# Performance work log

Measured on AMD Instinct MI355X. Metric: run time of the kernel, lower is better.

## Reference

```python
import jax, jax.numpy as jnp
import numpy as np

T, B, OBS, H, P, L, A = 512, 128, 512, 256, 128, 4, 4


def _ln(x, scale, bias, eps=1e-6):
    mu = jnp.mean(x, axis=-1, keepdims=True)
    var = jnp.mean((x - mu) ** 2, axis=-1, keepdims=True)
    return (x - mu) * jax.lax.rsqrt(var + eps) * scale + bias


def _binop(qi, qj):
    # S5 reset-aware associative operator: elements (A, b, reset_flag)
    Ai, bi, ci = qi
    Aj, bj, cj = qj
    A = (Aj * Ai) * (1.0 - cj) + Aj * cj
    b = (Aj * bi + bj) * (1.0 - cj) + bj * cj
    c = ci * (1.0 - cj) + cj
    return A, b, c


def _s5_layer(x, dones, h0, scale, bias, lam_re, lam_im, b_re, b_im, c_re, c_im, d_vec, log_step, glu_W, glu_b):
    # x: (T,B,H) real, dones: (T,B), h0: (B,P) complex64
    skip = x
    u = _ln(x, scale, bias)                                  # prenorm
    lam = lam_re + 1j * lam_im                               # (P,)
    step = jnp.exp(log_step)                                 # (P,)
    lam_bar = jnp.exp(lam * step)                            # ZOH discretization
    B_bar = ((lam_bar - 1.0) / lam)[:, None] * (b_re + 1j * b_im)  # (P,H)
    Bu = jnp.einsum('tbh,ph->tbp', u.astype(jnp.complex64), B_bar)  # (T,B,P)
    A_el = jnp.concatenate([jnp.ones((1, B, P), jnp.complex64),
                            jnp.broadcast_to(lam_bar.astype(jnp.complex64), (T, B, P))], axis=0)
    b_el = jnp.concatenate([h0[None], Bu], axis=0)
    c_el = jnp.concatenate([jnp.zeros((1, B, 1), jnp.float32), dones[..., None]], axis=0)
    _, xs, _ = jax.lax.associative_scan(_binop, (A_el, b_el, c_el), axis=0)
    xs = xs[1:]                                              # (T,B,P) complex states
    new_h = xs[-1]
    C = c_re + 1j * c_im                                     # (H,P)
    ys = 2.0 * jnp.real(jnp.einsum('tbp,hp->tbh', xs, C)) + d_vec * u  # conj_sym output + D*u
    z = _ln(ys, scale, bias)                                 # gtrxl norm (shared LayerNorm params)
    z = jax.nn.gelu(z)                                       # half_glu1
    z = z * jax.nn.sigmoid(z @ glu_W + glu_b)
    return skip + z, new_h


def setup_inputs() -> dict:
    key = jax.random.key(0)
    ks = jax.random.split(key, 40)
    f32 = jnp.float32

    def n(i, shape, s=1.0):
        return jax.random.normal(ks[i], shape, f32) * s

    inp = {}
    inp['obs'] = n(0, (T, B, OBS))
    inp['dones'] = (jax.random.uniform(ks[1], (T, B)) < 0.01).astype(f32)
    inp['hidden_re'] = jnp.zeros((L, B, P), f32)
    inp['hidden_im'] = jnp.zeros((L, B, P), f32)
    inp['enc0_W'] = n(2, (OBS, 128), 1.0 / np.sqrt(OBS))
    inp['enc0_b'] = jnp.zeros((128,), f32)
    inp['enc1_W'] = n(3, (128, H), 1.0 / np.sqrt(128))
    inp['enc1_b'] = jnp.zeros((H,), f32)
    inp['norm_scale'] = jnp.ones((L, H), f32)
    inp['norm_bias'] = jnp.zeros((L, H), f32)
    inp['Lambda_re'] = -0.5 * jax.random.uniform(ks[4], (L, P), f32) - 0.1
    inp['Lambda_im'] = n(5, (L, P), np.pi)
    inp['B_re'] = n(6, (L, P, H), 1.0 / np.sqrt(H))
    inp['B_im'] = n(7, (L, P, H), 1.0 / np.sqrt(H))
    inp['C_re'] = n(8, (L, H, P), 1.0 / np.sqrt(2 * P))
    inp['C_im'] = n(9, (L, H, P), 1.0 / np.sqrt(2 * P))
    inp['D'] = n(10, (L, H))
    inp['log_step'] = jax.random.uniform(ks[11], (L, P), f32, np.log(1e-3), np.log(1e-1))
    inp['glu_W'] = n(12, (L, H, H), 1.0 / np.sqrt(H))
    inp['glu_b'] = jnp.zeros((L, H), f32)
    inp['ab0_W'] = n(13, (H, 128), 1.0 / np.sqrt(H))
    inp['ab0_b'] = jnp.zeros((128,), f32)
    inp['ab1_W'] = n(14, (128, 128), 1.0 / np.sqrt(128))
    inp['ab1_b'] = jnp.zeros((128,), f32)
    inp['adec_W'] = n(15, (128, A), 0.01 / np.sqrt(128))
    inp['adec_b'] = jnp.full((A,), 0.5, f32)
    inp['log_std'] = jnp.full((A,), -0.7, f32)
    inp['vb0_W'] = n(16, (H, 128), 1.0 / np.sqrt(H))
    inp['vb0_b'] = jnp.zeros((128,), f32)
    inp['vb1_W'] = n(17, (128, 128), 1.0 / np.sqrt(128))
    inp['vb1_b'] = jnp.zeros((128,), f32)
    inp['vdec_W'] = n(18, (128, 1), 1.0 / np.sqrt(128))
    inp['vdec_b'] = jnp.zeros((1,), f32)
    return inp


def reference(obs, dones, hidden_re, hidden_im, enc0_W, enc0_b, enc1_W, enc1_b,
              norm_scale, norm_bias, Lambda_re, Lambda_im, B_re, B_im, C_re, C_im,
              D, log_step, glu_W, glu_b, ab0_W, ab0_b, ab1_W, ab1_b, adec_W, adec_b,
              log_std, vb0_W, vb0_b, vb1_W, vb1_b, vdec_W, vdec_b):
    e = jax.nn.leaky_relu(obs @ enc0_W + enc0_b)
    e = jax.nn.leaky_relu(e @ enc1_W + enc1_b)
    h0 = (hidden_re + 1j * hidden_im).astype(jnp.complex64)  # (L,B,P)
    new_h = []
    for l in range(L):
        e, hl = _s5_layer(e, dones, h0[l], norm_scale[l], norm_bias[l],
                          Lambda_re[l], Lambda_im[l], B_re[l], B_im[l],
                          C_re[l], C_im[l], D[l], log_step[l], glu_W[l], glu_b[l])
        new_h.append(hl)
    new_h = jnp.stack(new_h)
    am = jax.nn.leaky_relu(e @ ab0_W + ab0_b)
    am = jax.nn.leaky_relu(am @ ab1_W + ab1_b)
    am = am @ adec_W + adec_b                                # actor mean (T,B,A)
    v = jax.nn.leaky_relu(e @ vb0_W + vb0_b)
    v = jax.nn.leaky_relu(v @ vb1_W + vb1_b)
    v = v @ vdec_W + vdec_b                                  # critic (T,B,1)
    sc = jnp.broadcast_to(jnp.exp(log_std), am.shape)        # Normal scale (pi params)
    out = jnp.concatenate([am, sc, v], axis=-1)              # (T,B,2A+1)
    return out, jnp.real(new_h), jnp.imag(new_h)
```

## Files before the change

kernel.cpp:

```cpp
#include <hip/hip_runtime.h>
#include <math.h>

#define TT 512
#define BB 128
#define OBSD 512
#define HD 256
#define PD 128
#define LD 4
#define NTB (TT*BB)

typedef __bf16 bf16x8 __attribute__((ext_vector_type(8)));
typedef float  f32x4  __attribute__((ext_vector_type(4)));

__device__ __forceinline__ float bf2f(unsigned short u) {
    return __uint_as_float(((unsigned)u) << 16);
}
__device__ __forceinline__ unsigned short f2bf(float f) {
    unsigned u = __float_as_uint(f);
    unsigned r = (u + 0x7FFFu + ((u >> 16) & 1u)) >> 16;
    return (unsigned short)r;
}
__device__ __forceinline__ float gelu_f(float x) {
    float x3 = x * x * x;
    return 0.5f * x * (1.f + tanhf(0.7978845608028654f * (x + 0.044715f * x3)));
}

template<int MODE, int NJ, int NK>
__global__ __launch_bounds__(512) void mgemm2(
    const unsigned short* __restrict__ A, const unsigned short* __restrict__ BT,
    int LDA, const float* __restrict__ bias,
    const float* __restrict__ lnsc, const float* __restrict__ lnbi,
    const unsigned short* __restrict__ aux1, unsigned short* Xio,
    unsigned short* __restrict__ U, int wU)
{
    constexpr int NJW = NJ / 2;
    constexpr int LPS = 2 + NJW;
    constexpr int K = NK * 32;
    const int N = NJ * 64;
    __shared__ unsigned short smA[3 * 2048];
    __shared__ unsigned short smB[3 * NJ * 2048];
    float2 (*red)[8] = reinterpret_cast<float2(*)[8]>(&smA[0]);
    int tid = threadIdx.x;
    int lane = tid & 63, w = tid >> 6;
    int m16 = lane & 15, quad = lane >> 4;
    int m0 = blockIdx.x * 64;

    f32x4 acc[4][NJW] = {};

    auto stage = [&](int slot, int kt) {
        int k0 = kt << 5;
#pragma unroll
        for (int j = 0; j < 2; ++j) {
            int chunk = w * 2 + j;
            int e = chunk * 128 + lane * 2;
            int row = e >> 5, kb = e & 31;
            const unsigned short* g = A + (size_t)(m0 + row) * LDA + k0 + kb;
            __builtin_amdgcn_global_load_lds(
                (const __attribute__((address_space(1))) void*)g,
                (__attribute__((address_space(3))) void*)(smA + slot * 2048 + e), 4, 0, 0);
        }
#pragma unroll
        for (int j = 0; j < NJW; ++j) {
            int chunk = w * NJW + j;
            int e = chunk * 512 + lane * 8;
            int p = e >> 11, r = (e >> 5) & 63, kq = e & 31;
            const unsigned short* g = BT + (size_t)(p * 64 + r) * K + k0 + kq;
            __builtin_amdgcn_global_load_lds(
                (const __attribute__((address_space(1))) void*)g,
                (__attribute__((address_space(3))) void*)(smB + slot * NJ * 2048 + e), 16, 0, 0);
        }
    };

    int nk = NK;
    stage(0, 0);
    stage(1, 1);
    int cur = 0, nxt = 2;
    for (int t = 0; t < nk; ++t) {
        int rem = nk - 1 - t;
        if (rem >= 2) {
            stage(nxt, t + 2);
            nxt = (nxt == 2) ? 0 : nxt + 1;
            asm volatile("s_waitcnt vmcnt(%0)" :: "i"(2 * LPS) : "memory");
        } else if (rem == 1) {
            asm volatile("s_waitcnt vmcnt(%0)" :: "i"(LPS) : "memory");
        } else {
            asm volatile("s_waitcnt vmcnt(0)" ::: "memory");
        }
        __builtin_amdgcn_s_barrier();
        __builtin_amdgcn_sched_barrier(0);
        bf16x8 af[4], bfr[NJW];
#pragma unroll
        for (int mi = 0; mi < 4; ++mi)
            af[mi] = *(const bf16x8*)(smA + cur * 2048 + (mi * 16 + m16) * 32 + quad * 8);
#pragma unroll
        for (int nj = 0; nj < NJW; ++nj)
            bfr[nj] = *(const bf16x8*)(smB + cur * NJ * 2048 + (w * NJW + nj) * 512 + m16 * 32 + quad * 8);
#pragma unroll
        for (int mi = 0; mi < 4; ++mi)
#pragma unroll
            for (int nj = 0; nj < NJW; ++nj)
                acc[mi][nj] = __builtin_amdgcn_mfma_f32_16x16x32_bf16(
                    bfr[nj], af[mi], acc[mi][nj], 0, 0, 0);
        __builtin_amdgcn_sched_barrier(0);
        __builtin_amdgcn_s_barrier();
        cur = (cur == 2) ? 0 : cur + 1;
    }

    int colb = w * (NJW * 16) + quad * 4;

    if (MODE == 1) {
#pragma unroll
        for (int mi = 0; mi < 4; ++mi) {
            size_t rowb = (size_t)(m0 + mi * 16 + m16) * N;
#pragma unroll
            for (int nj = 0; nj < NJW; ++nj) {
                ushort4 o = { f2bf(acc[mi][nj][0]), f2bf(acc[mi][nj][1]),
                              f2bf(acc[mi][nj][2]), f2bf(acc[mi][nj][3]) };
                *(ushort4*)(U + rowb + colb + nj * 16) = o;
            }
        }
        return;
    }

#pragma unroll
    for (int mi = 0; mi < 4; ++mi) {
        size_t rowb = (size_t)(m0 + mi * 16 + m16) * N;
        float s = 0.f, q = 0.f;
#pragma unroll
        for (int nj = 0; nj < NJW; ++nj) {
            float4 bn = *(const float4*)(bias + colb + nj * 16);
            ushort4 a1, xo;
            if (MODE == 2 || MODE == 3) a1 = *(const ushort4*)(aux1 + rowb + colb + nj * 16);
            if (MODE == 3)              xo = *(const ushort4*)(Xio + rowb + colb + nj * 16);
            float vv[4];
#pragma unroll
            for (int r = 0; r < 4; ++r) {
                float v = acc[mi][nj][r];
                float bv = (r == 0) ? bn.x : (r == 1) ? bn.y : (r == 2) ? bn.z : bn.w;
                if (MODE == 0) {
                    v += bv; v = v > 0.f ? v : 0.01f * v;
                } else if (MODE == 2) {
                    float u = bf2f(r == 0 ? a1.x : r == 1 ? a1.y : r == 2 ? a1.z : a1.w);
                    v += bv * u;
                } else if (MODE == 3) {
                    float zz = bf2f(r == 0 ? a1.x : r == 1 ? a1.y : r == 2 ? a1.z : a1.w);
                    float xx = bf2f(r == 0 ? xo.x : r == 1 ? xo.y : r == 2 ? xo.z : xo.w);
                    float sg = 1.f / (1.f + expf(-(v + bv)));
                    v = xx + zz * sg;
                }
                vv[r] = v;
                acc[mi][nj][r] = v;
                s += v; q += v * v;
            }
            if (MODE == 0 || MODE == 3) {
                ushort4 o = { f2bf(vv[0]), f2bf(vv[1]), f2bf(vv[2]), f2bf(vv[3]) };
                *(ushort4*)(Xio + rowb + colb + nj * 16) = o;
            }
        }
        if (MODE != 3 || wU) {
            s += __shfl_xor(s, 16); q += __shfl_xor(q, 16);
            s += __shfl_xor(s, 32); q += __shfl_xor(q, 32);
            if (quad == 0) red[mi * 16 + m16][w] = float2{s, q};
        }
    }
    if (MODE == 3 && !wU) return;
    __syncthreads();

#pragma unroll
    for (int mi = 0; mi < 4; ++mi) {
        int row_l = mi * 16 + m16;
        float S = 0.f, Q = 0.f;
#pragma unroll
        for (int ww = 0; ww < 8; ++ww) {
            float2 tv = red[row_l][ww];
            S += tv.x; Q += tv.y;
        }
        float mu = S * (1.f / 256.f);
        float var = Q * (1.f / 256.f) - mu * mu;
        float rstd = rsqrtf(var + 1e-6f);
        size_t rowb = (size_t)(m0 + row_l) * N;
#pragma unroll
        for (int nj = 0; nj < NJW; ++nj) {
            float4 ls = *(const float4*)(lnsc + colb + nj * 16);
            float4 lb = *(const float4*)(lnbi + colb + nj * 16);
            float o[4];
#pragma unroll
            for (int r = 0; r < 4; ++r) {
                float sc = (r == 0) ? ls.x : (r == 1) ? ls.y : (r == 2) ? ls.z : ls.w;
                float bi = (r == 0) ? lb.x : (r == 1) ? lb.y : (r == 2) ? lb.z : lb.w;
                float v = (acc[mi][nj][r] - mu) * rstd * sc + bi;
                if (MODE == 2) v = gelu_f(v);
                o[r] = v;
            }
            ushort4 ov = { f2bf(o[0]), f2bf(o[1]), f2bf(o[2]), f2bf(o[3]) };
            *(ushort4*)(U + rowb + colb + nj * 16) = ov;
        }
    }
}

__global__ __launch_bounds__(512) void glu_bu_k(
    const unsigned short* __restrict__ Z,
    const unsigned short* __restrict__ GT,
    const unsigned short* __restrict__ BT2,
    const float* __restrict__ glub,
    const float* __restrict__ ns2, const float* __restrict__ nb2,
    unsigned short* __restrict__ Xio,
    unsigned short* __restrict__ Uo,
    unsigned short* __restrict__ BUo)
{
    const int N = 256;
    __shared__ unsigned short smA[2 * 2048];
    __shared__ unsigned short smB[2 * 8192];
    __shared__ unsigned short zbuf[64 * 264];
    float2 (*red)[8] = reinterpret_cast<float2(*)[8]>(&smA[0]);
    int tid = threadIdx.x;
    int lane = tid & 63, w = tid >> 6;
    int m16 = lane & 15, quad = lane >> 4;
    int m0 = blockIdx.x * 64;
    int colb = w * 32 + quad * 4;

    f32x4 acc[4][2] = {};

    auto stage1 = [&](int slot, int kt) {
        int k0 = kt << 5;
#pragma unroll
        for (int j = 0; j < 2; ++j) {
            int e = (w * 2 + j) * 128 + lane * 2;
            int row = e >> 5, kb = e & 31;
            const unsigned short* g = Z + (size_t)(m0 + row) * 256 + k0 + kb;
            __builtin_amdgcn_global_load_lds(
                (const __attribute__((address_space(1))) void*)g,
                (__attribute__((address_space(3))) void*)(smA + slot * 2048 + e), 4, 0, 0);
        }
#pragma unroll
        for (int j = 0; j < 2; ++j) {
            int e = (w * 2 + j) * 512 + lane * 8;
            int p = e >> 11, r = (e >> 5) & 63, kq = e & 31;
            const unsigned short* g = GT + (size_t)(p * 64 + r) * 256 + k0 + kq;
            __builtin_amdgcn_global_load_lds(
                (const __attribute__((address_space(1))) void*)g,
                (__attribute__((address_space(3))) void*)(smB + slot * 8192 + e), 16, 0, 0);
        }
    };
    auto stage2 = [&](int slot, int kt) {
        int k0 = kt << 5;
#pragma unroll
        for (int j = 0; j < 2; ++j) {
            int e = (w * 2 + j) * 512 + lane * 8;
            int p = e >> 11, r = (e >> 5) & 63, kq = e & 31;
            const unsigned short* g = BT2 + (size_t)(p * 64 + r) * 256 + k0 + kq;
            __builtin_amdgcn_global_load_lds(
                (const __attribute__((address_space(1))) void*)g,
                (__attribute__((address_space(3))) void*)(smB + slot * 8192 + e), 16, 0, 0);
        }
    };

    stage1(0, 0);
    for (int t = 0; t < 8; ++t) {
        int cur = t & 1;
        if (t + 1 < 8) {
            stage1(cur ^ 1, t + 1);
            asm volatile("s_waitcnt vmcnt(4)" ::: "memory");
        } else {
            asm volatile("s_waitcnt vmcnt(0)" ::: "memory");
        }
        __builtin_amdgcn_s_barrier();
        __builtin_amdgcn_sched_barrier(0);
        bf16x8 af[4], bfr[2];
#pragma unroll
        for (int mi = 0; mi < 4; ++mi)
            af[mi] = *(const bf16x8*)(smA + cur * 2048 + (mi * 16 + m16) * 32 + quad * 8);
#pragma unroll
        for (int nj = 0; nj < 2; ++nj)
            bfr[nj] = *(const bf16x8*)(smB + cur * 8192 + (w * 2 + nj) * 512 + m16 * 32 + quad * 8);
#pragma unroll
        for (int mi = 0; mi < 4; ++mi)
#pragma unroll
            for (int nj = 0; nj < 2; ++nj)
                acc[mi][nj] = __builtin_amdgcn_mfma_f32_16x16x32_bf16(
                    bfr[nj], af[mi], acc[mi][nj], 0, 0, 0);
        __builtin_amdgcn_sched_barrier(0);
        __builtin_amdgcn_s_barrier();
    }

    stage2(0, 0);

#pragma unroll
    for (int mi = 0; mi < 4; ++mi) {
        int row_l = mi * 16 + m16;
        size_t rowb = (size_t)(m0 + row_l) * N;
        float s = 0.f, q = 0.f;
#pragma unroll
        for (int nj = 0; nj < 2; ++nj) {
            float4 gb = *(const float4*)(glub + colb + nj * 16);
            ushort4 a1 = *(const ushort4*)(Z + rowb + colb + nj * 16);
            ushort4 xo = *(const ushort4*)(Xio + rowb + colb + nj * 16);
            float vv[4];
#pragma unroll
            for (int r = 0; r < 4; ++r) {
                float v = acc[mi][nj][r];
                float bv = (r == 0) ? gb.x : (r == 1) ? gb.y : (r == 2) ? gb.z : gb.w;
                float zz = bf2f(r == 0 ? a1.x : r == 1 ? a1.y : r == 2 ? a1.z : a1.w);
                float xx = bf2f(r == 0 ? xo.x : r == 1 ? xo.y : r == 2 ? xo.z : xo.w);
                float sg = 1.f / (1.f + expf(-(v + bv)));
                v = xx + zz * sg;
                vv[r] = v;
                acc[mi][nj][r] = v;
                s += v; q += v * v;
            }
            ushort4 o = { f2bf(vv[0]), f2bf(vv[1]), f2bf(vv[2]), f2bf(vv[3]) };
            *(ushort4*)(Xio + rowb + colb + nj * 16) = o;
        }
        s += __shfl_xor(s, 16); q += __shfl_xor(q, 16);
        s += __shfl_xor(s, 32); q += __shfl_xor(q, 32);
        if (quad == 0) red[row_l][w] = float2{s, q};
    }
    __syncthreads();

#pragma unroll
    for (int mi = 0; mi < 4; ++mi) {
        int row_l = mi * 16 + m16;
        float S = 0.f, Q = 0.f;
#pragma unroll
        for (int ww = 0; ww < 8; ++ww) { float2 tv = red[row_l][ww]; S += tv.x; Q += tv.y; }
        float mu = S * (1.f / 256.f);
        float var = Q * (1.f / 256.f) - mu * mu;
        float rstd = rsqrtf(var + 1e-6f);
        size_t rowb = (size_t)(m0 + row_l) * N;
#pragma unroll
        for (int nj = 0; nj < 2; ++nj) {
            float4 ls = *(const float4*)(ns2 + colb + nj * 16);
            float4 lb = *(const float4*)(nb2 + colb + nj * 16);
            float o[4];
#pragma unroll
            for (int r = 0; r < 4; ++r) {
                float sc = (r == 0) ? ls.x : (r == 1) ? ls.y : (r == 2) ? ls.z : ls.w;
                float bi = (r == 0) ? lb.x : (r == 1) ? lb.y : (r == 2) ? lb.z : lb.w;
                o[r] = (acc[mi][nj][r] - mu) * rstd * sc + bi;
            }
            ushort4 ov = { f2bf(o[0]), f2bf(o[1]), f2bf(o[2]), f2bf(o[3]) };
            *(ushort4*)(Uo + rowb + colb + nj * 16) = ov;
            *(ushort4*)(zbuf + row_l * 264 + colb + nj * 16) = ov;
        }
    }
    __syncthreads();

    f32x4 acc2[4][2] = {};
    for (int t = 0; t < 8; ++t) {
        int cur = t & 1;
        if (t + 1 < 8) {
            stage2(cur ^ 1, t + 1);
            asm volatile("s_waitcnt vmcnt(2)" ::: "memory");
        } else {
            asm volatile("s_waitcnt vmcnt(0)" ::: "memory");
        }
        __builtin_amdgcn_s_barrier();
        __builtin_amdgcn_sched_barrier(0);
        bf16x8 af[4], bfr[2];
#pragma unroll
        for (int mi = 0; mi < 4; ++mi)
            af[mi] = *(const bf16x8*)(zbuf + (mi * 16 + m16) * 264 + t * 32 + quad * 8);
#pragma unroll
        for (int nj = 0; nj < 2; ++nj)
            bfr[nj] = *(const bf16x8*)(smB + cur * 8192 + (w * 2 + nj) * 512 + m16 * 32 + quad * 8);
#pragma unroll
        for (int mi = 0; mi < 4; ++mi)
#pragma unroll
            for (int nj = 0; nj < 2; ++nj)
                acc2[mi][nj] = __builtin_amdgcn_mfma_f32_16x16x32_bf16(
                    bfr[nj], af[mi], acc2[mi][nj], 0, 0, 0);
        __builtin_amdgcn_sched_barrier(0);
        __builtin_amdgcn_s_barrier();
    }
#pragma unroll
    for (int mi = 0; mi < 4; ++mi) {
        size_t rowb = (size_t)(m0 + mi * 16 + m16) * N;
#pragma unroll
        for (int nj = 0; nj < 2; ++nj) {
            ushort4 o = { f2bf(acc2[mi][nj][0]), f2bf(acc2[mi][nj][1]),
                          f2bf(acc2[mi][nj][2]), f2bf(acc2[mi][nj][3]) };
            *(ushort4*)(BUo + rowb + colb + nj * 16) = o;
        }
    }
}

__global__ __launch_bounds__(512) void head_fused_k(
    const unsigned short* __restrict__ Xp, const unsigned short* __restrict__ W0T,
    const float* __restrict__ cb0,
    const unsigned short* __restrict__ AB1T, const unsigned short* __restrict__ VB1T,
    const float* __restrict__ ab1b, const float* __restrict__ vb1b,
    const float* __restrict__ adW, const float* __restrict__ adb,
    const float* __restrict__ lstd,
    const float* __restrict__ vdW, const float* __restrict__ vdb,
    float* __restrict__ out)
{
    __shared__ unsigned short smA[2 * 2048];
    __shared__ unsigned short smB[2 * 8192];
    __shared__ unsigned short zbuf[64 * 264];
    float (*redh)[8][4] = reinterpret_cast<float(*)[8][4]>(&smA[0]);
    int tid = threadIdx.x;
    int lane = tid & 63, w = tid >> 6;
    int m16 = lane & 15, quad = lane >> 4;
    int m0 = blockIdx.x * 64;
    int colb = w * 32 + quad * 4;

    f32x4 acc[4][2] = {};

    auto stage1 = [&](int slot, int kt) {
        int k0 = kt << 5;
#pragma unroll
        for (int j = 0; j < 2; ++j) {
            int e = (w * 2 + j) * 128 + lane * 2;
            int row = e >> 5, kb = e & 31;
            const unsigned short* g = Xp + (size_t)(m0 + row) * 256 + k0 + kb;
            __builtin_amdgcn_global_load_lds(
                (const __attribute__((address_space(1))) void*)g,
                (__attribute__((address_space(3))) void*)(smA + slot * 2048 + e), 4, 0, 0);
        }
#pragma unroll
        for (int j = 0; j < 2; ++j) {
            int e = (w * 2 + j) * 512 + lane * 8;
            int p = e >> 11, r = (e >> 5) & 63, kq = e & 31;
            const unsigned short* g = W0T + (size_t)(p * 64 + r) * 256 + k0 + kq;
            __builtin_amdgcn_global_load_lds(
                (const __attribute__((address_space(1))) void*)g,
                (__attribute__((address_space(3))) void*)(smB + slot * 8192 + e), 16, 0, 0);
        }
    };
    auto stage2 = [&](int slot, int kt) {
        int k0 = kt << 5;
#pragma unroll
        for (int j = 0; j < 2; ++j) {
            int e = (w * 2 + j) * 512 + lane * 8;
            int r = e >> 5, kq = e & 31;
            const unsigned short* g = (r < 128)
                ? AB1T + (size_t)r * 128 + k0 + kq
                : VB1T + (size_t)(r - 128) * 128 + k0 + kq;
            __builtin_amdgcn_global_load_lds(
                (const __attribute__((address_space(1))) void*)g,
                (__attribute__((address_space(3))) void*)(smB + slot * 8192 + e), 16, 0, 0);
        }
    };

    stage1(0, 0);
    for (int t = 0; t < 8; ++t) {
        int cur = t & 1;
        if (t + 1 < 8) {
            stage1(cur ^ 1, t + 1);
            asm volatile("s_waitcnt vmcnt(4)" ::: "memory");
        } else {
            asm volatile("s_waitcnt vmcnt(0)" ::: "memory");
        }
        __builtin_amdgcn_s_barrier();
        __builtin_amdgcn_sched_barrier(0);
        bf16x8 af[4], bfr[2];
#pragma unroll
        for (int mi = 0; mi < 4; ++mi)
            af[mi] = *(const bf16x8*)(smA + cur * 2048 + (mi * 16 + m16) * 32 + quad * 8);
#pragma unroll
        for (int nj = 0; nj < 2; ++nj)
            bfr[nj] = *(const bf16x8*)(smB + cur * 8192 + (w * 2 + nj) * 512 + m16 * 32 + quad * 8);
#pragma unroll
        for (int mi = 0; mi < 4; ++mi)
#pragma unroll
            for (int nj = 0; nj < 2; ++nj)
                acc[mi][nj] = __builtin_amdgcn_mfma_f32_16x16x32_bf16(
                    bfr[nj], af[mi], acc[mi][nj], 0, 0, 0);
        __builtin_amdgcn_sched_barrier(0);
        __builtin_amdgcn_s_barrier();
    }
    stage2(0, 0);
#pragma unroll
    for (int mi = 0; mi < 4; ++mi) {
        int row_l = mi * 16 + m16;
#pragma unroll
        for (int nj = 0; nj < 2; ++nj) {
            float4 bn = *(const float4*)(cb0 + colb + nj * 16);
            float v0 = acc[mi][nj][0] + bn.x; v0 = v0 > 0.f ? v0 : 0.01f * v0;
            float v1 = acc[mi][nj][1] + bn.y; v1 = v1 > 0.f ? v1 : 0.01f * v1;
            float v2 = acc[mi][nj][2] + bn.z; v2 = v2 > 0.f ? v2 : 0.01f * v2;
            float v3 = acc[mi][nj][3] + bn.w; v3 = v3 > 0.f ? v3 : 0.01f * v3;
            ushort4 o = { f2bf(v0), f2bf(v1), f2bf(v2), f2bf(v3) };
            *(ushort4*)(zbuf + row_l * 264 + colb + nj * 16) = o;
        }
    }
    __syncthreads();

    f32x4 acc2[4][2] = {};
    int abase = (w < 4) ? 0 : 128;
    for (int t = 0; t < 4; ++t) {
        int cur = t & 1;
        if (t + 1 < 4) {
            stage2(cur ^ 1, t + 1);
            asm volatile("s_waitcnt vmcnt(2)" ::: "memory");
        } else {
            asm volatile("s_waitcnt vmcnt(0)" ::: "memory");
        }
        __builtin_amdgcn_s_barrier();
        __builtin_amdgcn_sched_barrier(0);
        bf16x8 af[4], bfr[2];
#pragma unroll
        for (int mi = 0; mi < 4; ++mi)
            af[mi] = *(const bf16x8*)(zbuf + (mi * 16 + m16) * 264 + abase + t * 32 + quad * 8);
#pragma unroll
// ... 182 lines not shown
            float nhr = fmaf(s.x, hr, fmaf(-s.y, hi, s.z));
            float nhi = fmaf(s.x, hi, fmaf(s.y, hr, s.w));
            hr = nhr; hi = nhi;
        }
        outre[gid] = hr; outim[gid] = hi;
    }
    __syncthreads();
    float hr = shin[chunk][pl].x, hi = shin[chunk][pl].y;
#pragma unroll
    for (int j = 0; j < 32; ++j) {
        unsigned v = buf[j];
        float bur = bf2f((unsigned short)(v & 0xFFFFu));
        float bui = bf2f((unsigned short)(v >> 16));
        float nr, ni;
        if (sdone[t0 + j] != 0.f) { nr = bur; ni = bui; }
        else {
            nr = fmaf(ar, hr, fmaf(-ai, hi, bur));
            ni = fmaf(ar, hi, fmaf(ai, hr, bui));
        }
        hr = nr; hi = ni;
        size_t off = ((size_t)(t0 + j) * BB + b) * 256 + 2 * p;
        *(unsigned*)(xs + off) = ((unsigned)f2bf(ni) << 16) | f2bf(nr);
    }
}

__global__ __launch_bounds__(256) void prep_k(
    const float* __restrict__ Br, const float* __restrict__ Bi,
    const float* __restrict__ Cr, const float* __restrict__ Ci,
    const float* __restrict__ Lr, const float* __restrict__ Li,
    const float* __restrict__ ls, unsigned short* bbarT, unsigned short* ccatT)
{
    int gid = blockIdx.x * 256 + threadIdx.x;
    int l = gid >> 15;
    int rem = gid & 32767;
    int p = rem >> 8;
    int h = rem & 255;
    float lr = Lr[l * PD + p], li = Li[l * PD + p];
    float st = expf(ls[l * PD + p]);
    float er = expf(lr * st);
    float lbr = er * cosf(li * st);
    float lbi = er * sinf(li * st);
    float nr = lbr - 1.f, ni = lbi;
    float den = lr * lr + li * li;
    float fr = (nr * lr + ni * li) / den;
    float fi = (ni * lr - nr * li) / den;
    float bre = Br[(size_t)(l * PD + p) * HD + h];
    float bim = Bi[(size_t)(l * PD + p) * HD + h];
    size_t lb = (size_t)l * 65536;
    bbarT[lb + (size_t)(2 * p) * 256 + h]     = f2bf(fr * bre - fi * bim);
    bbarT[lb + (size_t)(2 * p + 1) * 256 + h] = f2bf(fr * bim + fi * bre);
    float cre = Cr[(size_t)(l * HD + h) * PD + p];
    float cim = Ci[(size_t)(l * HD + h) * PD + p];
    ccatT[lb + (size_t)h * 256 + 2 * p]     = f2bf(2.f * cre);
    ccatT[lb + (size_t)h * 256 + 2 * p + 1] = f2bf(-2.f * cim);
}

__global__ __launch_bounds__(256) void tcvt_k(const float* __restrict__ in,
    unsigned short* __restrict__ out, int K, int N)
{
    int gid = blockIdx.x * 256 + threadIdx.x;
    if (gid >= K * N) return;
    int k = gid / N, n = gid - k * N;
    out[(size_t)n * K + k] = f2bf(in[gid]);
}

__global__ __launch_bounds__(256) void tcvt4_k(const float* __restrict__ in,
    unsigned short* __restrict__ out)
{
    int gid = blockIdx.x * 256 + threadIdx.x;
    int l = gid >> 16;
    int rem = gid & 65535;
    int k = rem >> 8, n = rem & 255;
    out[(size_t)l * 65536 + (size_t)n * 256 + k] = f2bf(in[gid]);
}

__global__ __launch_bounds__(256) void catb_k(const float* __restrict__ a,
    const float* __restrict__ b, float* __restrict__ out)
{
    int i = threadIdx.x;
    out[i] = (i < 128) ? a[i] : b[i - 128];
}

extern "C" void kernel_launch(void* const* d_in, const int* in_sizes, int n_in,
                              void* d_out, int out_size, void* d_ws, size_t ws_size,
                              hipStream_t stream) {
    (void)in_sizes; (void)n_in; (void)out_size; (void)ws_size;
    const float* obs     = (const float*)d_in[0];
    const float* dones   = (const float*)d_in[1];
    const float* hre     = (const float*)d_in[2];
    const float* him     = (const float*)d_in[3];
    const float* enc0_W  = (const float*)d_in[4];
    const float* enc0_b  = (const float*)d_in[5];
    const float* enc1_W  = (const float*)d_in[6];
    const float* enc1_b  = (const float*)d_in[7];
    const float* nsc     = (const float*)d_in[8];
    const float* nbi     = (const float*)d_in[9];
    const float* Lre     = (const float*)d_in[10];
    const float* Lim     = (const float*)d_in[11];
    const float* B_re    = (const float*)d_in[12];
    const float* B_im    = (const float*)d_in[13];
    const float* C_re    = (const float*)d_in[14];
    const float* C_im    = (const float*)d_in[15];
    const float* Dv      = (const float*)d_in[16];
    const float* lstep   = (const float*)d_in[17];
    const float* glu_W   = (const float*)d_in[18];
    const float* glu_b   = (const float*)d_in[19];
    const float* ab0_W   = (const float*)d_in[20];
    const float* ab0_b   = (const float*)d_in[21];
    const float* ab1_W   = (const float*)d_in[22];
    const float* ab1_b   = (const float*)d_in[23];
    const float* adec_W  = (const float*)d_in[24];
    const float* adec_b  = (const float*)d_in[25];
    const float* log_std = (const float*)d_in[26];
    const float* vb0_W   = (const float*)d_in[27];
    const float* vb0_b   = (const float*)d_in[28];
    const float* vb1_W   = (const float*)d_in[29];
    const float* vb1_b   = (const float*)d_in[30];
    const float* vdec_W  = (const float*)d_in[31];
    const float* vdec_b  = (const float*)d_in[32];

    const size_t MB = (size_t)1 << 20;
    char* wsb = (char*)d_ws;
    unsigned short* XS    = (unsigned short*)(wsb);
    unsigned short* U1    = (unsigned short*)(wsb + 64 * MB);
    unsigned short* X     = (unsigned short*)(wsb + 96 * MB);
    unsigned short* U     = (unsigned short*)(wsb + 128 * MB);
    unsigned short* BU    = (unsigned short*)(wsb + 160 * MB);
    char* wgt = wsb + 192 * MB;
    unsigned short* BBART = (unsigned short*)(wgt);
    unsigned short* CCATT = (unsigned short*)(wgt + 512 * 1024);
    unsigned short* GLUT  = (unsigned short*)(wgt + 1024 * 1024);
    unsigned short* E0T   = (unsigned short*)(wgt + 1536 * 1024);
    unsigned short* E1T   = (unsigned short*)(wgt + 1664 * 1024);
    unsigned short* AB0VT = (unsigned short*)(wgt + 1728 * 1024);
    unsigned short* AB1T  = (unsigned short*)(wgt + 1856 * 1024);
    unsigned short* VB1T  = (unsigned short*)(wgt + 1888 * 1024);
    float*          CB0   = (float*)(wgt + 1920 * 1024);

    float* out   = (float*)d_out;
    float* outre = out + (size_t)NTB * 9;
    float* outim = outre + LD * BB * PD;

    prep_k<<<512, 256, 0, stream>>>(B_re, B_im, C_re, C_im, Lre, Lim, lstep, BBART, CCATT);
    tcvt_k<<<256, 256, 0, stream>>>(enc0_W, E0T, 512, 128);
    tcvt_k<<<128, 256, 0, stream>>>(enc1_W, E1T, 128, 256);
    tcvt4_k<<<1024, 256, 0, stream>>>(glu_W, GLUT);
    tcvt_k<<<128, 256, 0, stream>>>(ab0_W, AB0VT, 256, 128);
    tcvt_k<<<128, 256, 0, stream>>>(vb0_W, AB0VT + 128 * 256, 256, 128);
    tcvt_k<<<64, 256, 0, stream>>>(ab1_W, AB1T, 128, 128);
    tcvt_k<<<64, 256, 0, stream>>>(vb1_W, VB1T, 128, 128);
    catb_k<<<1, 256, 0, stream>>>(ab0_b, vb0_b, CB0);

    mgemm_obs<<<1024, 256, 0, stream>>>(obs, E0T, U1, enc0_b);
    mgemm2<0, 4, 4><<<1024, 512, 0, stream>>>(U1, E1T, 128, enc1_b, nsc, nbi, nullptr, X, U, 1);

    mgemm2<1, 4, 8><<<1024, 512, 0, stream>>>(U, BBART, 256,
                                           nullptr, nullptr, nullptr, nullptr, nullptr, BU, 0);
    for (int l = 0; l < LD; ++l) {
        scan2_k<<<512, 512, 0, stream>>>(BU, XS, dones, hre + l * BB * PD, him + l * BB * PD,
                                         Lre + l * PD, Lim + l * PD, lstep + l * PD,
                                         outre + l * BB * PD, outim + l * BB * PD);
        mgemm2<2, 4, 8><<<1024, 512, 0, stream>>>(XS, CCATT + (size_t)l * 65536, 256,
                                               Dv + l * HD, nsc + l * HD, nbi + l * HD, U, nullptr, U, 1);
        if (l + 1 < LD) {
            glu_bu_k<<<1024, 512, 0, stream>>>(U, GLUT + (size_t)l * 65536,
                                               BBART + (size_t)(l + 1) * 65536,
                                               glu_b + l * HD,
                                               nsc + (l + 1) * HD, nbi + (l + 1) * HD,
                                               X, U, BU);
        } else {
            mgemm2<3, 4, 8><<<1024, 512, 0, stream>>>(U, GLUT + (size_t)l * 65536, 256,
                                               glu_b + l * HD, nsc, nbi, U, X, U, 0);
        }
    }

    head_fused_k<<<1024, 512, 0, stream>>>(X, AB0VT, CB0, AB1T, VB1T, ab1_b, vb1_b,
                                           adec_W, adec_b, log_std, vdec_W, vdec_b, out);
}
```

Measured before the change: 872.4 us.

## Fuse C-projection, GLU and next-layer Bu GEMMs into one per-layer kernel

Each S5 layer now runs a single layer_k kernel that chains three GEMMs: the C output projection with D*u, LayerNorm and GELU, then the GLU gate with the residual, then the next layer's prenorm LayerNorm and the B_bar input projection. Intermediates stay in LDS (zbuf) between GEMMs instead of going through global memory. The encoder's second layer is fused the same way with the first Bu projection. This removes several kernel launches and a global round-trip of the normalized activations per layer, but each block now runs longer serial GEMM chains, which may lower occupancy because of the larger LDS footprint.

Result: slower. 927.0 us (+6.3%).

```diff
diff --git a/kernel.cpp b/kernel.cpp
--- a/kernel.cpp
+++ b/kernel.cpp
@@ -25,183 +25,16 @@
     return 0.5f * x * (1.f + tanhf(0.7978845608028654f * (x + 0.044715f * x3)));
 }
 
-template<int MODE, int NJ, int NK>
-__global__ __launch_bounds__(512) void mgemm2(
-    const unsigned short* __restrict__ A, const unsigned short* __restrict__ BT,
-    int LDA, const float* __restrict__ bias,
-    const float* __restrict__ lnsc, const float* __restrict__ lnbi,
-    const unsigned short* __restrict__ aux1, unsigned short* Xio,
-    unsigned short* __restrict__ U, int wU)
-{
-    constexpr int NJW = NJ / 2;
-    constexpr int LPS = 2 + NJW;
-    constexpr int K = NK * 32;
-    const int N = NJ * 64;
-    __shared__ unsigned short smA[3 * 2048];
-    __shared__ unsigned short smB[3 * NJ * 2048];
-    float2 (*red)[8] = reinterpret_cast<float2(*)[8]>(&smA[0]);
-    int tid = threadIdx.x;
-    int lane = tid & 63, w = tid >> 6;
-    int m16 = lane & 15, quad = lane >> 4;
-    int m0 = blockIdx.x * 64;
-
-    f32x4 acc[4][NJW] = {};
-
-    auto stage = [&](int slot, int kt) {
-        int k0 = kt << 5;
-#pragma unroll
-        for (int j = 0; j < 2; ++j) {
-            int chunk = w * 2 + j;
-            int e = chunk * 128 + lane * 2;
-            int row = e >> 5, kb = e & 31;
-            const unsigned short* g = A + (size_t)(m0 + row) * LDA + k0 + kb;
-            __builtin_amdgcn_global_load_lds(
-                (const __attribute__((address_space(1))) void*)g,
-                (__attribute__((address_space(3))) void*)(smA + slot * 2048 + e), 4, 0, 0);
-        }
-#pragma unroll
-        for (int j = 0; j < NJW; ++j) {
-            int chunk = w * NJW + j;
-            int e = chunk * 512 + lane * 8;
-            int p = e >> 11, r = (e >> 5) & 63, kq = e & 31;
-            const unsigned short* g = BT + (size_t)(p * 64 + r) * K + k0 + kq;
-            __builtin_amdgcn_global_load_lds(
-                (const __attribute__((address_space(1))) void*)g,
-                (__attribute__((address_space(3))) void*)(smB + slot * NJ * 2048 + e), 16, 0, 0);
-        }
-    };
-
-    int nk = NK;
-    stage(0, 0);
-    stage(1, 1);
-    int cur = 0, nxt = 2;
-    for (int t = 0; t < nk; ++t) {
-        int rem = nk - 1 - t;
-        if (rem >= 2) {
-            stage(nxt, t + 2);
-            nxt = (nxt == 2) ? 0 : nxt + 1;
-            asm volatile("s_waitcnt vmcnt(%0)" :: "i"(2 * LPS) : "memory");
-        } else if (rem == 1) {
-            asm volatile("s_waitcnt vmcnt(%0)" :: "i"(LPS) : "memory");
-        } else {
-            asm volatile("s_waitcnt vmcnt(0)" ::: "memory");
-        }
-        __builtin_amdgcn_s_barrier();
-        __builtin_amdgcn_sched_barrier(0);
-        bf16x8 af[4], bfr[NJW];
-#pragma unroll
-        for (int mi = 0; mi < 4; ++mi)
-            af[mi] = *(const bf16x8*)(smA + cur * 2048 + (mi * 16 + m16) * 32 + quad * 8);
-#pragma unroll
-        for (int nj = 0; nj < NJW; ++nj)
-            bfr[nj] = *(const bf16x8*)(smB + cur * NJ * 2048 + (w * NJW + nj) * 512 + m16 * 32 + quad * 8);
-#pragma unroll
-        for (int mi = 0; mi < 4; ++mi)
-#pragma unroll
-            for (int nj = 0; nj < NJW; ++nj)
-                acc[mi][nj] = __builtin_amdgcn_mfma_f32_16x16x32_bf16(
-                    bfr[nj], af[mi], acc[mi][nj], 0, 0, 0);
-        __builtin_amdgcn_sched_barrier(0);
-        __builtin_amdgcn_s_barrier();
-        cur = (cur == 2) ? 0 : cur + 1;
-    }
-
-    int colb = w * (NJW * 16) + quad * 4;
-
-    if (MODE == 1) {
-#pragma unroll
-        for (int mi = 0; mi < 4; ++mi) {
-            size_t rowb = (size_t)(m0 + mi * 16 + m16) * N;
-#pragma unroll
-            for (int nj = 0; nj < NJW; ++nj) {
-                ushort4 o = { f2bf(acc[mi][nj][0]), f2bf(acc[mi][nj][1]),
-                              f2bf(acc[mi][nj][2]), f2bf(acc[mi][nj][3]) };
-                *(ushort4*)(U + rowb + colb + nj * 16) = o;
-            }
-        }
-        return;
-    }
-
-#pragma unroll
-    for (int mi = 0; mi < 4; ++mi) {
-        size_t rowb = (size_t)(m0 + mi * 16 + m16) * N;
-        float s = 0.f, q = 0.f;
-#pragma unroll
-        for (int nj = 0; nj < NJW; ++nj) {
-            float4 bn = *(const float4*)(bias + colb + nj * 16);
-            ushort4 a1, xo;
-            if (MODE == 2 || MODE == 3) a1 = *(const ushort4*)(aux1 + rowb + colb + nj * 16);
-            if (MODE == 3)              xo = *(const ushort4*)(Xio + rowb + colb + nj * 16);
-            float vv[4];
-#pragma unroll
-            for (int r = 0; r < 4; ++r) {
-                float v = acc[mi][nj][r];
-                float bv = (r == 0) ? bn.x : (r == 1) ? bn.y : (r == 2) ? bn.z : bn.w;
-                if (MODE == 0) {
-                    v += bv; v = v > 0.f ? v : 0.01f * v;
-                } else if (MODE == 2) {
-                    float u = bf2f(r == 0 ? a1.x : r == 1 ? a1.y : r == 2 ? a1.z : a1.w);
-                    v += bv * u;
-                } else if (MODE == 3) {
-                    float zz = bf2f(r == 0 ? a1.x : r == 1 ? a1.y : r == 2 ? a1.z : a1.w);
-                    float xx = bf2f(r == 0 ? xo.x : r == 1 ? xo.y : r == 2 ? xo.z : xo.w);
-                    float sg = 1.f / (1.f + expf(-(v + bv)));
-                    v = xx + zz * sg;
-                }
-                vv[r] = v;
-                acc[mi][nj][r] = v;
-                s += v; q += v * v;
-            }
-            if (MODE == 0 || MODE == 3) {
-                ushort4 o = { f2bf(vv[0]), f2bf(vv[1]), f2bf(vv[2]), f2bf(vv[3]) };
-                *(ushort4*)(Xio + rowb + colb + nj * 16) = o;
-            }
-        }
-        if (MODE != 3 || wU) {
-            s += __shfl_xor(s, 16); q += __shfl_xor(q, 16);
-            s += __shfl_xor(s, 32); q += __shfl_xor(q, 32);
-            if (quad == 0) red[mi * 16 + m16][w] = float2{s, q};
-        }
-    }
-    if (MODE == 3 && !wU) return;
-    __syncthreads();
-
-#pragma unroll
-    for (int mi = 0; mi < 4; ++mi) {
-        int row_l = mi * 16 + m16;
-        float S = 0.f, Q = 0.f;
-#pragma unroll
-        for (int ww = 0; ww < 8; ++ww) {
-            float2 tv = red[row_l][ww];
-            S += tv.x; Q += tv.y;
-        }
-        float mu = S * (1.f / 256.f);
-        float var = Q * (1.f / 256.f) - mu * mu;
-        float rstd = rsqrtf(var + 1e-6f);
-        size_t rowb = (size_t)(m0 + row_l) * N;
-#pragma unroll
-        for (int nj = 0; nj < NJW; ++nj) {
-            float4 ls = *(const float4*)(lnsc + colb + nj * 16);
-            float4 lb = *(const float4*)(lnbi + colb + nj * 16);
-            float o[4];
-#pragma unroll
-            for (int r = 0; r < 4; ++r) {
-                float sc = (r == 0) ? ls.x : (r == 1) ? ls.y : (r == 2) ? ls.z : ls.w;
-                float bi = (r == 0) ? lb.x : (r == 1) ? lb.y : (r == 2) ? lb.z : lb.w;
-                float v = (acc[mi][nj][r] - mu) * rstd * sc + bi;
-                if (MODE == 2) v = gelu_f(v);
-                o[r] = v;
-            }
-            ushort4 ov = { f2bf(o[0]), f2bf(o[1]), f2bf(o[2]), f2bf(o[3]) };
-            *(ushort4*)(U + rowb + colb + nj * 16) = ov;
-        }
-    }
-}
-
-__global__ __launch_bounds__(512) void glu_bu_k(
-    const unsigned short* __restrict__ Z,
+
+template<int LAST>
+__global__ __launch_bounds__(512) void layer_k(
+    const unsigned short* __restrict__ XSp,
+    const unsigned short* __restrict__ Uaux,
+    const unsigned short* __restrict__ CT,
     const unsigned short* __restrict__ GT,
     const unsigned short* __restrict__ BT2,
+    const float* __restrict__ Dv,
+    const float* __restrict__ ns1, const float* __restrict__ nb1,
     const float* __restrict__ glub,
     const float* __restrict__ ns2, const float* __restrict__ nb2,
     unsigned short* __restrict__ Xio,
@@ -219,15 +52,13 @@
     int m0 = blockIdx.x * 64;
     int colb = w * 32 + quad * 4;
 
-    f32x4 acc[4][2] = {};
-
     auto stage1 = [&](int slot, int kt) {
         int k0 = kt << 5;
 #pragma unroll
         for (int j = 0; j < 2; ++j) {
             int e = (w * 2 + j) * 128 + lane * 2;
             int row = e >> 5, kb = e & 31;
-            const unsigned short* g = Z + (size_t)(m0 + row) * 256 + k0 + kb;
+            const unsigned short* g = XSp + (size_t)(m0 + row) * 256 + k0 + kb;
             __builtin_amdgcn_global_load_lds(
                 (const __attribute__((address_space(1))) void*)g,
                 (__attribute__((address_space(3))) void*)(smA + slot * 2048 + e), 4, 0, 0);
@@ -235,26 +66,27 @@
 #pragma unroll
         for (int j = 0; j < 2; ++j) {
             int e = (w * 2 + j) * 512 + lane * 8;
-            int p = e >> 11, r = (e >> 5) & 63, kq = e & 31;
-            const unsigned short* g = GT + (size_t)(p * 64 + r) * 256 + k0 + kq;
+            int r = e >> 5, kq = e & 31;
+            const unsigned short* g = CT + (size_t)r * 256 + k0 + kq;
             __builtin_amdgcn_global_load_lds(
                 (const __attribute__((address_space(1))) void*)g,
                 (__attribute__((address_space(3))) void*)(smB + slot * 8192 + e), 16, 0, 0);
         }
     };
-    auto stage2 = [&](int slot, int kt) {
+    auto stageB = [&](const unsigned short* BT, int slot, int kt) {
         int k0 = kt << 5;
 #pragma unroll
         for (int j = 0; j < 2; ++j) {
             int e = (w * 2 + j) * 512 + lane * 8;
-            int p = e >> 11, r = (e >> 5) & 63, kq = e & 31;
-            const unsigned short* g = BT2 + (size_t)(p * 64 + r) * 256 + k0 + kq;
+            int r = e >> 5, kq = e & 31;
+            const unsigned short* g = BT + (size_t)r * 256 + k0 + kq;
             __builtin_amdgcn_global_load_lds(
                 (const __attribute__((address_space(1))) void*)g,
                 (__attribute__((address_space(3))) void*)(smB + slot * 8192 + e), 16, 0, 0);
         }
     };
 
+    f32x4 acc[4][2] = {};
     stage1(0, 0);
     for (int t = 0; t < 8; ++t) {
         int cur = t & 1;
@@ -283,7 +115,7 @@
         __builtin_amdgcn_s_barrier();
     }
 
-    stage2(0, 0);
+    stageB(GT, 0, 0);
 
 #pragma unroll
     for (int mi = 0; mi < 4; ++mi) {
@@ -292,18 +124,279 @@
         float s = 0.f, q = 0.f;
 #pragma unroll
         for (int nj = 0; nj < 2; ++nj) {
+            float4 dn = *(const float4*)(Dv + colb + nj * 16);
+            ushort4 a1 = *(const ushort4*)(Uaux + rowb + colb + nj * 16);
+#pragma unroll
+            for (int r = 0; r < 4; ++r) {
+                float d = (r == 0) ? dn.x : (r == 1) ? dn.y : (r == 2) ? dn.z : dn.w;
+                float u = bf2f(r == 0 ? a1.x : r == 1 ? a1.y : r == 2 ? a1.z : a1.w);
+                float v = acc[mi][nj][r] + d * u;
+                acc[mi][nj][r] = v;
+                s += v; q += v * v;
+            }
+        }
+        s += __shfl_xor(s, 16); q += __shfl_xor(q, 16);
+        s += __shfl_xor(s, 32); q += __shfl_xor(q, 32);
+        if (quad == 0) red[row_l][w] = float2{s, q};
+    }
+    __syncthreads();
+#pragma unroll
+    for (int mi = 0; mi < 4; ++mi) {
+        int row_l = mi * 16 + m16;
+        float S = 0.f, Q = 0.f;
+#pragma unroll
+        for (int ww = 0; ww < 8; ++ww) { float2 tv = red[row_l][ww]; S += tv.x; Q += tv.y; }
+        float mu = S * (1.f / 256.f);
+        float var = Q * (1.f / 256.f) - mu * mu;
+        float rstd = rsqrtf(var + 1e-6f);
+#pragma unroll
+        for (int nj = 0; nj < 2; ++nj) {
+            float4 ls = *(const float4*)(ns1 + colb + nj * 16);
+            float4 lb = *(const float4*)(nb1 + colb + nj * 16);
+            float o[4];
+#pragma unroll
+            for (int r = 0; r < 4; ++r) {
+                float sc = (r == 0) ? ls.x : (r == 1) ? ls.y : (r == 2) ? ls.z : ls.w;
+                float bi = (r == 0) ? lb.x : (r == 1) ? lb.y : (r == 2) ? lb.z : lb.w;
+                o[r] = gelu_f((acc[mi][nj][r] - mu) * rstd * sc + bi);
+            }
+            ushort4 ov = { f2bf(o[0]), f2bf(o[1]), f2bf(o[2]), f2bf(o[3]) };
+            *(ushort4*)(zbuf + row_l * 264 + colb + nj * 16) = ov;
+        }
+    }
+    __syncthreads();
+
+    f32x4 acc2[4][2] = {};
+    for (int t = 0; t < 8; ++t) {
+        int cur = t & 1;
+        if (t + 1 < 8) {
+            stageB(GT, cur ^ 1, t + 1);
+            asm volatile("s_waitcnt vmcnt(2)" ::: "memory");
+        } else {
+            asm volatile("s_waitcnt vmcnt(0)" ::: "memory");
+        }
+        __builtin_amdgcn_s_barrier();
+        __builtin_amdgcn_sched_barrier(0);
+        bf16x8 af[4], bfr[2];
+#pragma unroll
+        for (int mi = 0; mi < 4; ++mi)
+            af[mi] = *(const bf16x8*)(zbuf + (mi * 16 + m16) * 264 + t * 32 + quad * 8);
+#pragma unroll
+        for (int nj = 0; nj < 2; ++nj)
+            bfr[nj] = *(const bf16x8*)(smB + cur * 8192 + (w * 2 + nj) * 512 + m16 * 32 + quad * 8);
+#pragma unroll
+        for (int mi = 0; mi < 4; ++mi)
+#pragma unroll
+            for (int nj = 0; nj < 2; ++nj)
+                acc2[mi][nj] = __builtin_amdgcn_mfma_f32_16x16x32_bf16(
+                    bfr[nj], af[mi], acc2[mi][nj], 0, 0, 0);
+        __builtin_amdgcn_sched_barrier(0);
+        __builtin_amdgcn_s_barrier();
+    }
+
+    if (!LAST) stageB(BT2, 0, 0);
+
+#pragma unroll
+    for (int mi = 0; mi < 4; ++mi) {
+        int row_l = mi * 16 + m16;
+        size_t rowb = (size_t)(m0 + row_l) * N;
+        float s = 0.f, q = 0.f;
+#pragma unroll
+        for (int nj = 0; nj < 2; ++nj) {
             float4 gb = *(const float4*)(glub + colb + nj * 16);
-            ushort4 a1 = *(const ushort4*)(Z + rowb + colb + nj * 16);
+            ushort4 zz = *(const ushort4*)(zbuf + row_l * 264 + colb + nj * 16);
             ushort4 xo = *(const ushort4*)(Xio + rowb + colb + nj * 16);
             float vv[4];
 #pragma unroll
             for (int r = 0; r < 4; ++r) {
+                float bv = (r == 0) ? gb.x : (r == 1) ? gb.y : (r == 2) ? gb.z : gb.w;
+                float zv = bf2f(r == 0 ? zz.x : r == 1 ? zz.y : r == 2 ? zz.z : zz.w);
+                float xv = bf2f(r == 0 ? xo.x : r == 1 ? xo.y : r == 2 ? xo.z : xo.w);
+                float sg = 1.f / (1.f + expf(-(acc2[mi][nj][r] + bv)));
+                float v = xv + zv * sg;
+                vv[r] = v;
+                acc2[mi][nj][r] = v;
+                s += v; q += v * v;
+            }
+            ushort4 o = { f2bf(vv[0]), f2bf(vv[1]), f2bf(vv[2]), f2bf(vv[3]) };
+            *(ushort4*)(Xio + rowb + colb + nj * 16) = o;
+        }
+        if (!LAST) {
+            s += __shfl_xor(s, 16); q += __shfl_xor(q, 16);
+            s += __shfl_xor(s, 32); q += __shfl_xor(q, 32);
+            if (quad == 0) red[row_l][w] = float2{s, q};
+        }
+    }
+    if (LAST) return;
+    __syncthreads();
+
+#pragma unroll
+    for (int mi = 0; mi < 4; ++mi) {
+        int row_l = mi * 16 + m16;
+        float S = 0.f, Q = 0.f;
+#pragma unroll
+        for (int ww = 0; ww < 8; ++ww) { float2 tv = red[row_l][ww]; S += tv.x; Q += tv.y; }
+        float mu = S * (1.f / 256.f);
+        float var = Q * (1.f / 256.f) - mu * mu;
+        float rstd = rsqrtf(var + 1e-6f);
+        size_t rowb = (size_t)(m0 + row_l) * N;
+#pragma unroll
+        for (int nj = 0; nj < 2; ++nj) {
+            float4 ls = *(const float4*)(ns2 + colb + nj * 16);
+            float4 lb = *(const float4*)(nb2 + colb + nj * 16);
+            float o[4];
+#pragma unroll
+            for (int r = 0; r < 4; ++r) {
+                float sc = (r == 0) ? ls.x : (r == 1) ? ls.y : (r == 2) ? ls.z : ls.w;
+                float bi = (r == 0) ? lb.x : (r == 1) ? lb.y : (r == 2) ? lb.z : lb.w;
+                o[r] = (acc2[mi][nj][r] - mu) * rstd * sc + bi;
+            }
+            ushort4 ov = { f2bf(o[0]), f2bf(o[1]), f2bf(o[2]), f2bf(o[3]) };
+            *(ushort4*)(Uo + rowb + colb + nj * 16) = ov;
+            *(ushort4*)(zbuf + row_l * 264 + colb + nj * 16) = ov;
+        }
+    }
+    __syncthreads();
+
+    f32x4 acc3[4][2] = {};
+    for (int t = 0; t < 8; ++t) {
+        int cur = t & 1;
+        if (t + 1 < 8) {
+            stageB(BT2, cur ^ 1, t + 1);
+            asm volatile("s_waitcnt vmcnt(2)" ::: "memory");
+        } else {
+            asm volatile("s_waitcnt vmcnt(0)" ::: "memory");
+        }
+        __builtin_amdgcn_s_barrier();
+        __builtin_amdgcn_sched_barrier(0);
+        bf16x8 af[4], bfr[2];
+#pragma unroll
+        for (int mi = 0; mi < 4; ++mi)
+            af[mi] = *(const bf16x8*)(zbuf + (mi * 16 + m16) * 264 + t * 32 + quad * 8);
+#pragma unroll
+        for (int nj = 0; nj < 2; ++nj)
+            bfr[nj] = *(const bf16x8*)(smB + cur * 8192 + (w * 2 + nj) * 512 + m16 * 32 + quad * 8);
+#pragma unroll
+        for (int mi = 0; mi < 4; ++mi)
+#pragma unroll
+            for (int nj = 0; nj < 2; ++nj)
+                acc3[mi][nj] = __builtin_amdgcn_mfma_f32_16x16x32_bf16(
+                    bfr[nj], af[mi], acc3[mi][nj], 0, 0, 0);
+        __builtin_amdgcn_sched_barrier(0);
+        __builtin_amdgcn_s_barrier();
+    }
+#pragma unroll
+    for (int mi = 0; mi < 4; ++mi) {
+        size_t rowb = (size_t)(m0 + mi * 16 + m16) * N;
+#pragma unroll
+        for (int nj = 0; nj < 2; ++nj) {
+            ushort4 o = { f2bf(acc3[mi][nj][0]), f2bf(acc3[mi][nj][1]),
+                          f2bf(acc3[mi][nj][2]), f2bf(acc3[mi][nj][3]) };
+            *(ushort4*)(BUo + rowb + colb + nj * 16) = o;
+        }
+    }
+}
+
+__global__ __launch_bounds__(512) void enc1_bu_k(
+    const unsigned short* __restrict__ U1p,
+    const unsigned short* __restrict__ E1T,
+    const unsigned short* __restrict__ BT0,
+    const float* __restrict__ e1b,
+    const float* __restrict__ ns0, const float* __restrict__ nb0,
+    unsigned short* __restrict__ Xio,
+    unsigned short* __restrict__ Uo,
+    unsigned short* __restrict__ BUo)
+{
+    const int N = 256;
+    __shared__ unsigned short smA[2 * 2048];
+    __shared__ unsigned short smB[2 * 8192];
+    __shared__ unsigned short zbuf[64 * 264];
+    float2 (*red)[8] = reinterpret_cast<float2(*)[8]>(&smA[0]);
+    int tid = threadIdx.x;
+    int lane = tid & 63, w = tid >> 6;
+    int m16 = lane & 15, quad = lane >> 4;
+    int m0 = blockIdx.x * 64;
+    int colb = w * 32 + quad * 4;
+
+    auto stage1 = [&](int slot, int kt) {
+        int k0 = kt << 5;
+#pragma unroll
+        for (int j = 0; j < 2; ++j) {
+            int e = (w * 2 + j) * 128 + lane * 2;
+            int row = e >> 5, kb = e & 31;
+            const unsigned short* g = U1p + (size_t)(m0 + row) * 128 + k0 + kb;
+            __builtin_amdgcn_global_load_lds(
+                (const __attribute__((address_space(1))) void*)g,
+                (__attribute__((address_space(3))) void*)(smA + slot * 2048 + e), 4, 0, 0);
+        }
+#pragma unroll
+        for (int j = 0; j < 2; ++j) {
+            int e = (w * 2 + j) * 512 + lane * 8;
+            int r = e >> 5, kq = e & 31;
+            const unsigned short* g = E1T + (size_t)r * 128 + k0 + kq;
+            __builtin_amdgcn_global_load_lds(
+                (const __attribute__((address_space(1))) void*)g,
+                (__attribute__((address_space(3))) void*)(smB + slot * 8192 + e), 16, 0, 0);
+        }
+    };
+    auto stageB = [&](int slot, int kt) {
+        int k0 = kt << 5;
+#pragma unroll
+        for (int j = 0; j < 2; ++j) {
+            int e = (w * 2 + j) * 512 + lane * 8;
+            int r = e >> 5, kq = e & 31;
+            const unsigned short* g = BT0 + (size_t)r * 256 + k0 + kq;
+            __builtin_amdgcn_global_load_lds(
+                (const __attribute__((address_space(1))) void*)g,
+                (__attribute__((address_space(3))) void*)(smB + slot * 8192 + e), 16, 0, 0);
+        }
+    };
+
+    f32x4 acc[4][2] = {};
+    stage1(0, 0);
+    for (int t = 0; t < 4; ++t) {
+        int cur = t & 1;
+        if (t + 1 < 4) {
+            stage1(cur ^ 1, t + 1);
+            asm volatile("s_waitcnt vmcnt(4)" ::: "memory");
+        } else {
+            asm volatile("s_waitcnt vmcnt(0)" ::: "memory");
+        }
+        __builtin_amdgcn_s_barrier();
+        __builtin_amdgcn_sched_barrier(0);
+        bf16x8 af[4], bfr[2];
+#pragma unroll
+        for (int mi = 0; mi < 4; ++mi)
+            af[mi] = *(const bf16x8*)(smA + cur * 2048 + (mi * 16 + m16) * 32 + quad * 8);
+#pragma unroll
+        for (int nj = 0; nj < 2; ++nj)
+            bfr[nj] = *(const bf16x8*)(smB + cur * 8192 + (w * 2 + nj) * 512 + m16 * 32 + quad * 8);
+#pragma unroll
+        for (int mi = 0; mi < 4; ++mi)
+#pragma unroll
+            for (int nj = 0; nj < 2; ++nj)
+                acc[mi][nj] = __builtin_amdgcn_mfma_f32_16x16x32_bf16(
+                    bfr[nj], af[mi], acc[mi][nj], 0, 0, 0);
+        __builtin_amdgcn_sched_barrier(0);
+        __builtin_amdgcn_s_barrier();
+    }
+
+    stageB(0, 0);
+
+#pragma unroll
+    for (int mi = 0; mi < 4; ++mi) {
+        int row_l = mi * 16 + m16;
+        size_t rowb = (size_t)(m0 + row_l) * N;
+        float s = 0.f, q = 0.f;
+#pragma unroll
+        for (int nj = 0; nj < 2; ++nj) {
+            float4 bn = *(const float4*)(e1b + colb + nj * 16);
+            float vv[4];
+#pragma unroll
+            for (int r = 0; r < 4; ++r) {
                 float v = acc[mi][nj][r];
-                float bv = (r == 0) ? gb.x : (r == 1) ? gb.y : (r == 2) ? gb.z : gb.w;
-                float zz = bf2f(r == 0 ? a1.x : r == 1 ? a1.y : r == 2 ? a1.z : a1.w);
-                float xx = bf2f(r == 0 ? xo.x : r == 1 ? xo.y : r == 2 ? xo.z : xo.w);
-                float sg = 1.f / (1.f + expf(-(v + bv)));
-                v = xx + zz * sg;
+                float bv = (r == 0) ? bn.x : (r == 1) ? bn.y : (r == 2) ? bn.z : bn.w;
+                v += bv; v = v > 0.f ? v : 0.01f * v;
                 vv[r] = v;
                 acc[mi][nj][r] = v;
                 s += v; q += v * v;
@@ -316,7 +409,6 @@
         if (quad == 0) red[row_l][w] = float2{s, q};
     }
     __syncthreads();
-
 #pragma unroll
     for (int mi = 0; mi < 4; ++mi) {
         int row_l = mi * 16 + m16;
@@ -329,8 +421,8 @@
         size_t rowb = (size_t)(m0 + row_l) * N;
 #pragma unroll
         for (int nj = 0; nj < 2; ++nj) {
-            float4 ls = *(const float4*)(ns2 + colb + nj * 16);
-            float4 lb = *(const float4*)(nb2 + colb + nj * 16);
+            float4 ls = *(const float4*)(ns0 + colb + nj * 16);
+            float4 lb = *(const float4*)(nb0 + colb + nj * 16);
             float o[4];
 #pragma unroll
             for (int r = 0; r < 4; ++r) {
@@ -349,7 +441,7 @@
     for (int t = 0; t < 8; ++t) {
         int cur = t & 1;
         if (t + 1 < 8) {
-            stage2(cur ^ 1, t + 1);
+            stageB(cur ^ 1, t + 1);
             asm volatile("s_waitcnt vmcnt(2)" ::: "memory");
         } else {
             asm volatile("s_waitcnt vmcnt(0)" ::: "memory");
@@ -838,25 +930,23 @@
     catb_k<<<1, 256, 0, stream>>>(ab0_b, vb0_b, CB0);
 
     mgemm_obs<<<1024, 256, 0, stream>>>(obs, E0T, U1, enc0_b);
-    mgemm2<0, 4, 4><<<1024, 512, 0, stream>>>(U1, E1T, 128, enc1_b, nsc, nbi, nullptr, X, U, 1);
-
-    mgemm2<1, 4, 8><<<1024, 512, 0, stream>>>(U, BBART, 256,
-                                           nullptr, nullptr, nullptr, nullptr, nullptr, BU, 0);
+    enc1_bu_k<<<1024, 512, 0, stream>>>(U1, E1T, BBART, enc1_b, nsc, nbi, X, U, BU);
+
     for (int l = 0; l < LD; ++l) {
         scan2_k<<<512, 512, 0, stream>>>(BU, XS, dones, hre + l * BB * PD, him + l * BB * PD,
                                          Lre + l * PD, Lim + l * PD, lstep + l * PD,
                                          outre + l * BB * PD, outim + l * BB * PD);
-        mgemm2<2, 4, 8><<<1024, 512, 0, stream>>>(XS, CCATT + (size_t)l * 65536, 256,
-                                               Dv + l * HD, nsc + l * HD, nbi + l * HD, U, nullptr, U, 1);
         if (l + 1 < LD) {
-            glu_bu_k<<<1024, 512, 0, stream>>>(U, GLUT + (size_t)l * 65536,
-                                               BBART + (size_t)(l + 1) * 65536,
-                                               glu_b + l * HD,
-                                               nsc + (l + 1) * HD, nbi + (l + 1) * HD,
-                                               X, U, BU);
+            layer_k<0><<<1024, 512, 0, stream>>>(XS, U,
+                CCATT + (size_t)l * 65536, GLUT + (size_t)l * 65536,
+                BBART + (size_t)(l + 1) * 65536,
+                Dv + l * HD, nsc + l * HD, nbi + l * HD, glu_b + l * HD,
+                nsc + (l + 1) * HD, nbi + (l + 1) * HD, X, U, BU);
         } else {
-            mgemm2<3, 4, 8><<<1024, 512, 0, stream>>>(U, GLUT + (size_t)l * 65536, 256,
-                                               glu_b + l * HD, nsc, nbi, U, X, U, 0);
+            layer_k<1><<<1024, 512, 0, stream>>>(XS, U,
+                CCATT + (size_t)l * 65536, GLUT + (size_t)l * 65536, nullptr,
+                Dv + l * HD, nsc + l * HD, nbi + l * HD, glu_b + l * HD,
+                nullptr, nullptr, X, nullptr, nullptr);
         }
     }
 
```
